# Performance work log

Measured on AMD Instinct MI355X. Metric: run time of the kernel, lower is better.

## Reference

```python
import jax, jax.numpy as jnp
import numpy as np

N_NODES = 100000
N_EDGES = 1600000
C = 64       # in_channels == filters
K = 3        # Chebyshev order
EPS = 1e-5   # InstanceNorm eps


def setup_inputs() -> dict:
    key = jax.random.key(0)
    ks = jax.random.split(key, 8)
    x = jax.random.normal(ks[0], (N_NODES, C), dtype=jnp.float32)
    edge_index = jax.random.randint(ks[1], (2, N_EDGES), 0, N_NODES, dtype=jnp.int64)
    scale = 1.0 / np.sqrt(C)
    W1 = jax.random.normal(ks[2], (K, C, C), dtype=jnp.float32) * scale
    b1 = jnp.zeros((C,), dtype=jnp.float32)
    W2 = jax.random.normal(ks[3], (K, C, C), dtype=jnp.float32) * scale
    b2 = jnp.zeros((C,), dtype=jnp.float32)
    return {"x": x, "edge_index": edge_index, "W1": W1, "b1": b1, "W2": W2, "b2": b2}


def _cheb_conv(x, src, dst, w_edge, W, b, n):
    # PyG ChebConv, norm='sym', lambda_max=2: L_hat = -D^{-1/2} A D^{-1/2}
    def prop(h):  # h: [N, C] -> L_hat @ h via gather -> weight -> scatter-add
        return jax.ops.segment_sum(w_edge[:, None] * h[src], dst, num_segments=n)
    Tx0 = x
    Tx1 = prop(x)
    Tx2 = 2.0 * prop(Tx1) - Tx0
    return Tx0 @ W[0] + Tx1 @ W[1] + Tx2 @ W[2] + b


def _instance_norm(h):
    # PyG InstanceNorm (single graph, affine=False): normalize over nodes per channel
    m = h.mean(axis=0, keepdims=True)
    v = h.var(axis=0, keepdims=True)
    return (h - m) * jax.lax.rsqrt(v + EPS)


def reference(x, edge_index, W1, b1, W2, b2):
    n = x.shape[0]
    src, dst = edge_index[0], edge_index[1]
    ones = jnp.ones((src.shape[0],), dtype=x.dtype)
    deg = jax.ops.segment_sum(ones, dst, num_segments=n)
    safe = jnp.where(deg > 0, deg, 1.0)
    dinv = jnp.where(deg > 0, jax.lax.rsqrt(safe), 0.0)
    w_edge = -dinv[src] * dinv[dst]  # scaled-Laplacian edge weights
    h = _instance_norm(jax.nn.relu(_cheb_conv(x, src, dst, w_edge, W1, b1, n)))
    h = _instance_norm(jax.nn.relu(_cheb_conv(h, src, dst, w_edge, W2, b2, n)))
    return h
```

## Files before the change

kernel.cpp:

```cpp
#include <hip/hip_runtime.h>
#include <hip/hip_fp16.h>

#define NCH 64
#define EPS 1e-5f
#define SBANKS 32
#define BSHIFT 8
#define NHIST 256
#define BINCAP 3200
#define NBINMIN 512
#define PADRES 2048
#define RSHIFT 14
#define SRCMASK 0x1FFFFu
#define QW_SCALE 32767.0f
#define QW_INV (1.0f/32767.0f)

typedef _Float16 f16x8 __attribute__((ext_vector_type(8)));
typedef float f32x4 __attribute__((ext_vector_type(4)));

__global__ __launch_bounds__(256) void k_front(const float* __restrict__ x, __half* __restrict__ xh,
                                               int castTotal, int castB,
                                               const float* __restrict__ W1, _Float16* __restrict__ Wb1,
                                               const float* __restrict__ W2, _Float16* __restrict__ Wb2,
                                               const int* __restrict__ dst, int* __restrict__ cnt,
                                               int E, int per, int nbuck) {
    int bid = blockIdx.x;
    if (bid < castB) {
        int i = (bid * 256 + threadIdx.x) * 4;
        if (i < castTotal) {
            float4 f = *(const float4*)(x + i);
            __half2* o = (__half2*)(xh + i);
            o[0] = __floats2half2_rn(f.x, f.y);
            o[1] = __floats2half2_rn(f.z, f.w);
        }
        return;
    }
    if (bid < castB + 96) {
        int wb = bid - castB;
        const float* W = (wb < 48) ? W1 : W2;
        _Float16* Wb = (wb < 48) ? Wb1 : Wb2;
        int idx = (wb % 48) * 256 + threadIdx.x;
        int j = idx & 7;
        int lane = (idx >> 3) & 63;
        int tk = idx >> 9;
        int tile = tk / 6, kk = tk % 6;
        int k = kk * 32 + (lane >> 4) * 8 + j;
        int n = tile * 16 + (lane & 15);
        Wb[idx] = (_Float16)W[k * 64 + n];
        return;
    }
    __shared__ int lh[512];
    int hb = bid - castB - 96;
    for (int t = threadIdx.x; t < nbuck; t += 256) lh[t] = 0;
    __syncthreads();
    int lo = hb * per, hi = min(E, lo + per);
    for (int e = lo + threadIdx.x; e < hi; e += 256)
        atomicAdd(&lh[dst[e] >> BSHIFT], 1);
    __syncthreads();
    for (int t = threadIdx.x; t < nbuck; t += 256)
        if (lh[t]) atomicAdd(&cnt[t], lh[t]);
}

__global__ void k_bscan(const int* __restrict__ cnt, int* __restrict__ gbase,
                        int* __restrict__ gcur, int nbuck, int E) {
    __shared__ int s[512];
    int t = threadIdx.x;
    int v = (t < nbuck) ? cnt[t] : 0;
    s[t] = v;
    __syncthreads();
    for (int off = 1; off < 512; off <<= 1) {
        int add = (t >= off) ? s[t - off] : 0;
        __syncthreads();
        s[t] += add;
        __syncthreads();
    }
    if (t < nbuck) { int ex = s[t] - v; gbase[t] = ex; gcur[t] = ex; }
    if (t == 0) gbase[nbuck] = E;
}

__global__ __launch_bounds__(256) void k_bin(const int* __restrict__ src,
                                             const int* __restrict__ dst,
                                             int* __restrict__ gcur,
                                             int2* __restrict__ binned, int E, int per, int nbuck) {
    __shared__ int lh[512];
    __shared__ int lsc[512];
    __shared__ int lbase[512];
    __shared__ int lcur[512];
    __shared__ int2 sedge[BINCAP];
    int t = threadIdx.x;
    for (int i = t; i < 512; i += 256) lh[i] = 0;
    __syncthreads();
    int lo = blockIdx.x * per, hi = min(E, lo + per);
    for (int e = lo + t; e < hi; e += 256)
        atomicAdd(&lh[dst[e] >> BSHIFT], 1);
    __syncthreads();
    int v0 = lh[t], v1 = lh[t + 256];
    lsc[t] = v0; lsc[t + 256] = v1;
    __syncthreads();
    for (int off = 1; off < 512; off <<= 1) {
        int a0 = (t >= off) ? lsc[t - off] : 0;
        int a1 = (t + 256 >= off) ? lsc[t + 256 - off] : 0;
        __syncthreads();
        lsc[t] += a0; lsc[t + 256] += a1;
        __syncthreads();
    }
    lsc[t] -= v0; lsc[t + 256] -= v1;
    if (t < nbuck && v0) lbase[t] = atomicAdd(&gcur[t], v0);
    if (t + 256 < nbuck && v1) lbase[t + 256] = atomicAdd(&gcur[t + 256], v1);
    lcur[t] = lsc[t]; lcur[t + 256] = lsc[t + 256];
    __syncthreads();
    for (int e = lo + t; e < hi; e += 256) {
        int d = dst[e];
        int b = d >> BSHIFT;
        int pos = atomicAdd(&lcur[b], 1);
        sedge[pos] = make_int2(src[e], d);
    }
    __syncthreads();
    int cntE = hi - lo;
    for (int i = t; i < cntE; i += 256) {
        int2 sd = sedge[i];
        int b = sd.y >> BSHIFT;
        binned[lbase[b] + (i - lsc[b])] = sd;
    }
}

__global__ __launch_bounds__(256) void k_bucket(const int2* __restrict__ binned,
                                                const int* __restrict__ gbase,
                                                float* __restrict__ dinv,
                                                int2* __restrict__ rowinfo,
                                                unsigned int* __restrict__ csr, int N, int nbuck) {
    __shared__ int hist8[256 * 8];
    __shared__ int cur8[256 * 8];
    __shared__ int ldeg[256];
    __shared__ int ltmp[256];
    int b = blockIdx.x;
    int t = threadIdx.x;
    int nodeLo = b << BSHIFT;
    int nHere = min(256, N - nodeLo);
    int e0 = gbase[b], e1 = gbase[b + 1];
    int pb = (gbase[b] + b * PADRES + 7) & ~7;
    for (int i = t; i < 256 * 8; i += 256) hist8[i] = 0;
    __syncthreads();
    for (int e = e0 + t; e < e1; e += 256) {
        int2 sd = binned[e];
        atomicAdd(&hist8[((sd.y - nodeLo) << 3) + (sd.x >> RSHIFT)], 1);
    }
    __syncthreads();
    int c[8], deg = 0;
#pragma unroll
    for (int r = 0; r < 8; r++) { c[r] = hist8[(t << 3) + r]; deg += c[r]; }
    int pdeg = (deg + 7) & ~7;
    ldeg[t] = deg;
    if (t < nHere) dinv[nodeLo + t] = (deg > 0) ? rsqrtf((float)deg) : 0.0f;
    ltmp[t] = pdeg;
    __syncthreads();
    for (int off = 1; off < 256; off <<= 1) {
        int add = (t >= off) ? ltmp[t - off] : 0;
        __syncthreads();
        ltmp[t] += add;
        __syncthreads();
    }
    int lstart = ltmp[t] - pdeg;
    if (t < nHere) rowinfo[nodeLo + t] = make_int2(pb + lstart, pdeg);
    int run = lstart;
#pragma unroll
    for (int r = 0; r < 8; r++) { cur8[(t << 3) + r] = run; run += c[r]; }
    __syncthreads();
    for (int e = e0 + t; e < e1; e += 256) {
        int2 sd = binned[e];
        int dl = sd.y - nodeLo;
        int pos = atomicAdd(&cur8[(dl << 3) + (sd.x >> RSHIFT)], 1);
        unsigned int dd = (unsigned int)min(ldeg[dl], 32767);
        csr[pb + pos] = (unsigned int)sd.x | (dd << 17);
    }
    __syncthreads();
    if (t < nHere) {
        int d = ldeg[t];
        int pd = (d + 7) & ~7;
        if (pd > d) {
            unsigned int fill = (d > 0) ? (csr[pb + lstart] & SRCMASK) : 0u;
            for (int i = d; i < pd; i++) csr[pb + lstart + i] = fill;
        }
    }
}

__global__ void k_weights(unsigned int* __restrict__ csr, const float* __restrict__ dinv, int PE) {
    int e = blockIdx.x * blockDim.x + threadIdx.x;
    if (e < PE) {
        unsigned int v = csr[e];
        unsigned int d = v >> 17;
        if (d == 0) return;
        unsigned int s = v & SRCMASK;
        float aw = dinv[s] * rsqrtf((float)d);
        unsigned int qw = (unsigned int)(aw * QW_SCALE + 0.5f);
        csr[e] = s | (qw << 17);
    }
}


#define GATH(A0,A1,A2,A3,A4,A5,A6,A7, C0, C1) \
    A0 = *(const uint4*)(hb + (size_t)(C0.x & SRCMASK) * NCH); \
    A1 = *(const uint4*)(hb + (size_t)(C0.y & SRCMASK) * NCH); \
    A2 = *(const uint4*)(hb + (size_t)(C0.z & SRCMASK) * NCH); \
    A3 = *(const uint4*)(hb + (size_t)(C0.w & SRCMASK) * NCH); \
    A4 = *(const uint4*)(hb + (size_t)(C1.x & SRCMASK) * NCH); \
    A5 = *(const uint4*)(hb + (size_t)(C1.y & SRCMASK) * NCH); \
    A6 = *(const uint4*)(hb + (size_t)(C1.z & SRCMASK) * NCH); \
    A7 = *(const uint4*)(hb + (size_t)(C1.w & SRCMASK) * NCH);

#define FMA1(A, W) { \
    float2 f; \
    f = __half22float2(*(const __half2*)&A.x); acc[0] = fmaf(W, f.x, acc[0]); acc[1] = fmaf(W, f.y, acc[1]); \
    f = __half22float2(*(const __half2*)&A.y); acc[2] = fmaf(W, f.x, acc[2]); acc[3] = fmaf(W, f.y, acc[3]); \
    f = __half22float2(*(const __half2*)&A.z); acc[4] = fmaf(W, f.x, acc[4]); acc[5] = fmaf(W, f.y, acc[5]); \
    f = __half22float2(*(const __half2*)&A.w); acc[6] = fmaf(W, f.x, acc[6]); acc[7] = fmaf(W, f.y, acc[7]); }

#define FMA8(A0,A1,A2,A3,A4,A5,A6,A7, C0, C1) { \
    float w0 = -(float)(C0.x >> 17) * QW_INV; \
    float w1 = -(float)(C0.y >> 17) * QW_INV; \
    float w2 = -(float)(C0.z >> 17) * QW_INV; \
    float w3 = -(float)(C0.w >> 17) * QW_INV; \
    float w4 = -(float)(C1.x >> 17) * QW_INV; \
    float w5 = -(float)(C1.y >> 17) * QW_INV; \
    float w6 = -(float)(C1.z >> 17) * QW_INV; \
    float w7 = -(float)(C1.w >> 17) * QW_INV; \
    sw += ((w0 + w1) + (w2 + w3)) + ((w4 + w5) + (w6 + w7)); \
    FMA1(A0, w0) FMA1(A1, w1) FMA1(A2, w2) FMA1(A3, w3) \
    FMA1(A4, w4) FMA1(A5, w5) FMA1(A6, w6) FMA1(A7, w7) }

__global__ __launch_bounds__(256) void k_prop(const __half* __restrict__ h,
                                              const int2* __restrict__ rowinfo,
                                              const unsigned int* __restrict__ csr,
                                              const __half* __restrict__ tx0,
                                              __half* __restrict__ y, int N,
                                              const float* __restrict__ gbank,
                                              const float* __restrict__ tbank,
                                              float invN) {
    __shared__ float sm[64], sr[64];
    const float* bank = (gbank != nullptr) ? gbank : tbank;
    if (bank != nullptr) {
        int tt = threadIdx.x;
        if (tt < 64) {
            float S = 0.f, Q = 0.f;
            for (int k = 0; k < SBANKS; k++) {
                S += bank[k * 128 + tt];
                Q += bank[k * 128 + 64 + tt];
            }
            float m = S * invN;
            float var = Q * invN - m * m;
            sm[tt] = m;
            sr[tt] = rsqrtf(var + EPS);
        }
        __syncthreads();
    }
    int lane = threadIdx.x & 63;
    int wv = (blockIdx.x * 256 + threadIdx.x) >> 6;
    int g = lane >> 3, li = lane & 7;
    int node = wv * 8 + g;
    int e = 0, e1 = 0;
    if (node < N) {
        int2 info = rowinfo[node];
        e = info.x;
        e1 = info.x + info.y;
    }
    float acc[8] = {0.f, 0.f, 0.f, 0.f, 0.f, 0.f, 0.f, 0.f};
    float sw = 0.0f;
    const __half* hb = h + li * 8;
    uint4 c0, c1;
    if (e < e1) {
        c0 = *(const uint4*)(csr + e);
        c1 = *(const uint4*)(csr + e + 4);
    }
    for (; e < e1; e += 8) {
        int en = (e + 8 < e1) ? (e + 8) : e;
        uint4 n0 = *(const uint4*)(csr + en);
        uint4 n1 = *(const uint4*)(csr + en + 4);
        uint4 a0, a1, a2, a3, a4, a5, a6, a7;
        GATH(a0, a1, a2, a3, a4, a5, a6, a7, c0, c1);
        FMA8(a0, a1, a2, a3, a4, a5, a6, a7, c0, c1);
        c0 = n0; c1 = n1;
    }
    if (node >= N) return;
    if (gbank != nullptr) {
        float4 m0 = *(const float4*)(sm + li * 8);
        float4 m1 = *(const float4*)(sm + li * 8 + 4);
        float4 r0 = *(const float4*)(sr + li * 8);
        float4 r1 = *(const float4*)(sr + li * 8 + 4);
        acc[0] = r0.x * (acc[0] - m0.x * sw);
        acc[1] = r0.y * (acc[1] - m0.y * sw);
        acc[2] = r0.z * (acc[2] - m0.z * sw);
        acc[3] = r0.w * (acc[3] - m0.w * sw);
        acc[4] = r1.x * (acc[4] - m1.x * sw);
        acc[5] = r1.y * (acc[5] - m1.y * sw);
        acc[6] = r1.z * (acc[6] - m1.z * sw);
        acc[7] = r1.w * (acc[7] - m1.w * sw);
    }
    if (tx0 != nullptr) {
        uint4 tq = *(const uint4*)(tx0 + (size_t)node * NCH + li * 8);
        float tv[8];
        float2 f;
        f = __half22float2(*(__half2*)&tq.x); tv[0] = f.x; tv[1] = f.y;
        f = __half22float2(*(__half2*)&tq.y); tv[2] = f.x; tv[3] = f.y;
        f = __half22float2(*(__half2*)&tq.z); tv[4] = f.x; tv[5] = f.y;
        f = __half22float2(*(__half2*)&tq.w); tv[6] = f.x; tv[7] = f.y;
        if (tbank != nullptr) {
            float4 m0 = *(const float4*)(sm + li * 8);
            float4 m1 = *(const float4*)(sm + li * 8 + 4);
            float4 r0 = *(const float4*)(sr + li * 8);
            float4 r1 = *(const float4*)(sr + li * 8 + 4);
            tv[0] = (tv[0] - m0.x) * r0.x; tv[1] = (tv[1] - m0.y) * r0.y;
            tv[2] = (tv[2] - m0.z) * r0.z; tv[3] = (tv[3] - m0.w) * r0.w;
            tv[4] = (tv[4] - m1.x) * r1.x; tv[5] = (tv[5] - m1.y) * r1.y;
            tv[6] = (tv[6] - m1.z) * r1.z; tv[7] = (tv[7] - m1.w) * r1.w;
        }
#pragma unroll
        for (int j = 0; j < 8; j++) acc[j] = 2.0f * acc[j] - tv[j];
    }
    uint4 o;
    __half2 hh;
    hh = __floats2half2_rn(acc[0], acc[1]); o.x = *(unsigned int*)&hh;
    hh = __floats2half2_rn(acc[2], acc[3]); o.y = *(unsigned int*)&hh;
    hh = __floats2half2_rn(acc[4], acc[5]); o.z = *(unsigned int*)&hh;
    hh = __floats2half2_rn(acc[6], acc[7]); o.w = *(unsigned int*)&hh;
    *(uint4*)(y + (size_t)node * NCH + li * 8) = o;
}

template <typename TOUT>
__global__ __launch_bounds__(256) void k_dmm(const __half* __restrict__ tx0,
                                             const __half* __restrict__ tx1,
                                             const __half* __restrict__ tx2,
                                             const _Float16* __restrict__ Wb,
                                             const float* __restrict__ b,
                                             TOUT* __restrict__ out,
                                             float* __restrict__ statsP, int N,
                                             const float* __restrict__ tbank,
                                             float invN) {
    __shared__ float sred[64];
    __shared__ float sq[64];
    __shared__ float tm[64];
    __shared__ float tr[64];
    int t = threadIdx.x;
    int w = t >> 6;
    int lane = t & 63;
    if (t < 64) {
        sred[t] = 0.f; sq[t] = 0.f;
        if (tbank != nullptr) {
            float S = 0.f, Q = 0.f;
            for (int k = 0; k < SBANKS; k++) {
                S += tbank[k * 128 + t];
                Q += tbank[k * 128 + 64 + t];
            }
            float m = S * invN;
            float var = Q * invN - m * m;
            tm[t] = m;
            tr[t] = rsqrtf(var + EPS);
        }
    }
    __syncthreads();

    int nb16 = blockIdx.x * 64 + w * 16;
    int m = lane & 15, q = lane >> 4;
    int row = nb16 + m;
    int rowC = (row < N) ? row : 0;
    const __half* base0 = tx0 + (size_t)rowC * NCH;
    const __half* base1 = tx1 + (size_t)rowC * NCH;
    const __half* base2 = tx2 + (size_t)rowC * NCH;

    f32x4 acc[4];
#pragma unroll
    for (int tile = 0; tile < 4; tile++) acc[tile] = (f32x4){0.f, 0.f, 0.f, 0.f};

#pragma unroll
    for (int kk = 0; kk < 6; kk++) {
        const __half* ap = (kk < 2 ? base0 : (kk < 4 ? base1 : base2)) + (kk & 1) * 32 + q * 8;
        f16x8 a = *(const f16x8*)ap;
        if (kk < 2 && tbank != nullptr) {
            int cbase = (kk & 1) * 32 + q * 8;
#pragma unroll
            for (int j = 0; j < 8; j++) {
                float v = (float)a[j];
                a[j] = (_Float16)((v - tm[cbase + j]) * tr[cbase + j]);
            }
        }
#pragma unroll
        for (int tile = 0; tile < 4; tile++) {
            f16x8 bf = *(const f16x8*)(Wb + ((size_t)(tile * 6 + kk) * 64 + lane) * 8);
            acc[tile] = __builtin_amdgcn_mfma_f32_16x16x32_f16(a, bf, acc[tile], 0, 0, 0);
        }
    }

#pragma unroll
    for (int tile = 0; tile < 4; tile++) {
        int ch = tile * 16 + m;
        float bb = b[ch];
        float s = 0.f, qq = 0.f;
#pragma unroll
        for (int r = 0; r < 4; r++) {
            int node = nb16 + q * 4 + r;
            float v = fmaxf(acc[tile][r] + bb, 0.f);
            if (node < N) {
                out[(size_t)node * NCH + ch] = (TOUT)v;
                s += v;
                qq = fmaf(v, v, qq);
            }
        }
        s += __shfl_xor(s, 16, 64);  s += __shfl_xor(s, 32, 64);
        qq += __shfl_xor(qq, 16, 64); qq += __shfl_xor(qq, 32, 64);
        if (q == 0) { atomicAdd(&sred[ch], s); atomicAdd(&sq[ch], qq); }
    }
    __syncthreads();
    if (t < 64) {
        int bank = blockIdx.x & (SBANKS - 1);
        atomicAdd(&statsP[bank * 128 + t], sred[t]);
        atomicAdd(&statsP[bank * 128 + 64 + t], sq[t]);
    }
}

__global__ __launch_bounds__(256) void k_norm_hf(const __half* __restrict__ a, float* __restrict__ o,
                                                 const float* __restrict__ sbank, float invN,
                                                 int total8) {
    __shared__ float sm[64];
    __shared__ float sr[64];
    int t = threadIdx.x;
    if (t < 64) {
        float S = 0.f, Q = 0.f;
        for (int k = 0; k < SBANKS; k++) {
            S += sbank[k * 128 + t];
            Q += sbank[k * 128 + 64 + t];
        }
        float m = S * invN;
        float var = Q * invN - m * m;
        sm[t] = m;
        sr[t] = rsqrtf(var + EPS);
    }
    __syncthreads();
    int i = blockIdx.x * 256 + t;
    if (i >= total8) return;
    int c0 = (i & 7) * 8;
    float4 m0 = *(const float4*)(sm + c0);
    float4 m1 = *(const float4*)(sm + c0 + 4);
    float4 r0 = *(const float4*)(sr + c0);
    float4 r1 = *(const float4*)(sr + c0 + 4);
    uint4 q = *(const uint4*)(a + (size_t)i * 8);
    float2 f;
    float4 o0, o1;
    f = __half22float2(*(__half2*)&q.x); o0.x = (f.x - m0.x) * r0.x; o0.y = (f.y - m0.y) * r0.y;
    f = __half22float2(*(__half2*)&q.y); o0.z = (f.x - m0.z) * r0.z; o0.w = (f.y - m0.w) * r0.w;
    f = __half22float2(*(__half2*)&q.z); o1.x = (f.x - m1.x) * r1.x; o1.y = (f.y - m1.y) * r1.y;
    f = __half22float2(*(__half2*)&q.w); o1.z = (f.x - m1.z) * r1.z; o1.w = (f.y - m1.w) * r1.w;
    *(float4*)(o + (size_t)i * 8) = o0;
    *(float4*)(o + (size_t)i * 8 + 4) = o1;
}

extern "C" void kernel_launch(void* const* d_in, const int* in_sizes, int n_in,
                              void* d_out, int out_size, void* d_ws, size_t ws_size,
                              hipStream_t stream) {
    const float* x  = (const float*)d_in[0];
    const int*   ei = (const int*)d_in[1];
    const float* W1 = (const float*)d_in[2];
    const float* b1 = (const float*)d_in[3];
    const float* W2 = (const float*)d_in[4];
    const float* b2 = (const float*)d_in[5];
    float* out = (float*)d_out;

    const int N = in_sizes[0] / NCH;
    const int E = in_sizes[1] / 2;
    const int* src = ei;
    const int* dst = ei + E;
    const int nbuck = (N + 255) >> BSHIFT;
    const int PE = E + nbuck * PADRES + 8;

    char* p = (char*)d_ws;
    auto alloc = [&](size_t bytes) {
        void* r = (void*)p;
        p += ((bytes + 255) / 256) * 256;
        return r;
    };
    float*  dinv     = (float*)alloc((size_t)131072 * 4);
    int2*   rowinfo  = (int2*)alloc((size_t)N * 8);
    unsigned int* csr = (unsigned int*)alloc((size_t)PE * 4);
    __half* xh       = (__half*)alloc((size_t)N * NCH * 2);
    __half* Tx1      = (__half*)alloc((size_t)N * NCH * 2);
    __half* Tx2      = (__half*)alloc((size_t)N * NCH * 2);
    __half* A        = (__half*)alloc((size_t)N * NCH * 2);
    __half* A2       = (__half*)alloc((size_t)N * NCH * 2);
    _Float16* Wb1    = (_Float16*)alloc(12288 * 2);
    _Float16* Wb2    = (_Float16*)alloc(12288 * 2);
    int*    gbase    = (int*)alloc((size_t)(nbuck + 1) * 4);
    int*    gcur     = (int*)alloc((size_t)nbuck * 4);
    const int statsFloats = SBANKS * 128 + 128;
    int*    cnt      = (int*)alloc((size_t)nbuck * 4 + (size_t)2 * statsFloats * 4);
    float*  stats1   = (float*)(cnt + nbuck);
    float*  stats2   = stats1 + statsFloats;

    int2* binned = (int2*)Tx1;

    hipMemsetAsync(cnt, 0, (size_t)nbuck * 4 + (size_t)2 * statsFloats * 4, stream);

    const int TB = 256;
    int nbin = (E + BINCAP - 1) / BINCAP;
    if (nbin < NBINMIN) nbin = NBINMIN;
    const int perBin = (E + nbin - 1) / nbin;
    const int perH = (E + NHIST - 1) / NHIST;
    const int castTotal = N * NCH;
    const int castB = (castTotal / 4 + TB - 1) / TB;
    k_front<<<castB + 96 + NHIST, TB, 0, stream>>>(x, xh, castTotal, castB,
                                                   W1, Wb1, W2, Wb2,
                                                   dst, cnt, E, perH, nbuck);
    k_bscan<<<1, 512, 0, stream>>>(cnt, gbase, gcur, nbuck, E);
    k_bin<<<nbin, TB, 0, stream>>>(src, dst, gcur, binned, E, perBin, nbuck);
    k_bucket<<<nbuck, TB, 0, stream>>>(binned, gbase, dinv, rowinfo, csr, N, nbuck);
    k_weights<<<(PE + TB - 1) / TB, TB, 0, stream>>>(csr, dinv, PE);

    const int propWaves = (N + 7) / 8;
    const int propBlocks = (propWaves + 3) / 4;
    const int dmmBlocks = (N + 63) / 64;
    const int total8 = (N * NCH) / 8;
    const int normBlocks = (total8 + TB - 1) / TB;
    const float invN = 1.0f / (float)N;

    k_prop<<<propBlocks, TB, 0, stream>>>(xh, rowinfo, csr, nullptr, Tx1, N, nullptr, nullptr, invN);
    k_prop<<<propBlocks, TB, 0, stream>>>(Tx1, rowinfo, csr, xh, Tx2, N, nullptr, nullptr, invN);
    k_dmm<__half><<<dmmBlocks, TB, 0, stream>>>(xh, Tx1, Tx2, Wb1, b1, A, stats1, N, nullptr, invN);

    k_prop<<<propBlocks, TB, 0, stream>>>(A, rowinfo, csr, nullptr, Tx1, N, stats1, nullptr, invN);
    k_prop<<<propBlocks, TB, 0, stream>>>(Tx1, rowinfo, csr, A, Tx2, N, nullptr, stats1, invN);
    k_dmm<__half><<<dmmBlocks, TB, 0, stream>>>(A, Tx1, Tx2, Wb2, b2, A2, stats2, N, stats1, invN);
    k_norm_hf<<<normBlocks, TB, 0, stream>>>(A2, out, stats2, invN, total8);
}
```

Before: 324.5 us.

## Compute degrees in binning pass and fold edge-weight quantization into bucket kernel

The binning kernel now counts per-node degree with global atomics, and a small kernel turns the degrees into dinv before bucketing. The bucket kernel then writes quantized edge weights straight into the CSR, which removes the separate full pass over the padded edge array. Binning also drops its shared-memory staging and prefix scan: it uses a fixed 1024 blocks and scatters edges directly with local atomic cursors. The costs are global atomics on a degree array, a larger memset, and less coalesced writes to the binned array.

After: 395.6 us. 1.22x slower.

```diff
diff --git a/kernel.cpp b/kernel.cpp
--- a/kernel.cpp
+++ b/kernel.cpp
@@ -6,8 +6,7 @@
 #define SBANKS 32
 #define BSHIFT 8
 #define NHIST 256
-#define BINCAP 3200
-#define NBINMIN 512
+#define NBIN 1024
 #define PADRES 2048
 #define RSHIFT 14
 #define SRCMASK 0x1FFFFu
@@ -80,57 +79,49 @@
 __global__ __launch_bounds__(256) void k_bin(const int* __restrict__ src,
                                              const int* __restrict__ dst,
                                              int* __restrict__ gcur,
+                                             int* __restrict__ deg,
                                              int2* __restrict__ binned, int E, int per, int nbuck) {
     __shared__ int lh[512];
-    __shared__ int lsc[512];
     __shared__ int lbase[512];
-    __shared__ int lcur[512];
-    __shared__ int2 sedge[BINCAP];
     int t = threadIdx.x;
-    for (int i = t; i < 512; i += 256) lh[i] = 0;
+    lh[t] = 0; lh[t + 256] = 0;
     __syncthreads();
     int lo = blockIdx.x * per, hi = min(E, lo + per);
-    for (int e = lo + t; e < hi; e += 256)
-        atomicAdd(&lh[dst[e] >> BSHIFT], 1);
-    __syncthreads();
-    int v0 = lh[t], v1 = lh[t + 256];
-    lsc[t] = v0; lsc[t + 256] = v1;
-    __syncthreads();
-    for (int off = 1; off < 512; off <<= 1) {
-        int a0 = (t >= off) ? lsc[t - off] : 0;
-        int a1 = (t + 256 >= off) ? lsc[t + 256 - off] : 0;
-        __syncthreads();
-        lsc[t] += a0; lsc[t + 256] += a1;
-        __syncthreads();
-    }
-    lsc[t] -= v0; lsc[t + 256] -= v1;
-    if (t < nbuck && v0) lbase[t] = atomicAdd(&gcur[t], v0);
-    if (t + 256 < nbuck && v1) lbase[t + 256] = atomicAdd(&gcur[t + 256], v1);
-    lcur[t] = lsc[t]; lcur[t + 256] = lsc[t + 256];
+    for (int e = lo + t; e < hi; e += 256) {
+        int d = dst[e];
+        atomicAdd(&lh[d >> BSHIFT], 1);
+        atomicAdd(&deg[d], 1);
+    }
+    __syncthreads();
+    int c0 = lh[t], c1 = lh[t + 256];
+    if (c0) lbase[t] = atomicAdd(&gcur[t], c0);
+    if (c1) lbase[t + 256] = atomicAdd(&gcur[t + 256], c1);
+    lh[t] = 0; lh[t + 256] = 0;
     __syncthreads();
     for (int e = lo + t; e < hi; e += 256) {
         int d = dst[e];
         int b = d >> BSHIFT;
-        int pos = atomicAdd(&lcur[b], 1);
-        sedge[pos] = make_int2(src[e], d);
-    }
-    __syncthreads();
-    int cntE = hi - lo;
-    for (int i = t; i < cntE; i += 256) {
-        int2 sd = sedge[i];
-        int b = sd.y >> BSHIFT;
-        binned[lbase[b] + (i - lsc[b])] = sd;
+        int pos = atomicAdd(&lh[b], 1);
+        binned[lbase[b] + pos] = make_int2(src[e], d);
+    }
+}
+
+__global__ void k_dinv(const int* __restrict__ deg, float* __restrict__ dinv, int N) {
+    int i = blockIdx.x * blockDim.x + threadIdx.x;
+    if (i < N) {
+        int d = deg[i];
+        dinv[i] = (d > 0) ? rsqrtf((float)d) : 0.0f;
     }
 }
 
 __global__ __launch_bounds__(256) void k_bucket(const int2* __restrict__ binned,
                                                 const int* __restrict__ gbase,
-                                                float* __restrict__ dinv,
+                                                const float* __restrict__ dinv,
                                                 int2* __restrict__ rowinfo,
                                                 unsigned int* __restrict__ csr, int N, int nbuck) {
     __shared__ int hist8[256 * 8];
     __shared__ int cur8[256 * 8];
-    __shared__ int ldeg[256];
+    __shared__ float ldr[256];
     __shared__ int ltmp[256];
     int b = blockIdx.x;
     int t = threadIdx.x;
@@ -149,8 +140,7 @@
 #pragma unroll
     for (int r = 0; r < 8; r++) { c[r] = hist8[(t << 3) + r]; deg += c[r]; }
     int pdeg = (deg + 7) & ~7;
-    ldeg[t] = deg;
-    if (t < nHere) dinv[nodeLo + t] = (deg > 0) ? rsqrtf((float)deg) : 0.0f;
+    ldr[t] = (deg > 0) ? rsqrtf((float)deg) : 0.0f;
     ltmp[t] = pdeg;
     __syncthreads();
     for (int off = 1; off < 256; off <<= 1) {
@@ -169,30 +159,20 @@
         int2 sd = binned[e];
         int dl = sd.y - nodeLo;
         int pos = atomicAdd(&cur8[(dl << 3) + (sd.x >> RSHIFT)], 1);
-        unsigned int dd = (unsigned int)min(ldeg[dl], 32767);
-        csr[pb + pos] = (unsigned int)sd.x | (dd << 17);
+        float aw = dinv[sd.x] * ldr[dl];
+        unsigned int qw = (unsigned int)(aw * QW_SCALE + 0.5f);
+        csr[pb + pos] = (unsigned int)sd.x | (qw << 17);
     }
     __syncthreads();
     if (t < nHere) {
-        int d = ldeg[t];
+        int d = 0;
+#pragma unroll
+        for (int r = 0; r < 8; r++) d += c[r];
         int pd = (d + 7) & ~7;
         if (pd > d) {
             unsigned int fill = (d > 0) ? (csr[pb + lstart] & SRCMASK) : 0u;
             for (int i = d; i < pd; i++) csr[pb + lstart + i] = fill;
         }
-    }
-}
-
-__global__ void k_weights(unsigned int* __restrict__ csr, const float* __restrict__ dinv, int PE) {
-    int e = blockIdx.x * blockDim.x + threadIdx.x;
-    if (e < PE) {
-        unsigned int v = csr[e];
-        unsigned int d = v >> 17;
-        if (d == 0) return;
-        unsigned int s = v & SRCMASK;
-        float aw = dinv[s] * rsqrtf((float)d);
-        unsigned int qw = (unsigned int)(aw * QW_SCALE + 0.5f);
-        csr[e] = s | (qw << 17);
     }
 }
 
@@ -475,7 +455,7 @@
         p += ((bytes + 255) / 256) * 256;
         return r;
     };
-    float*  dinv     = (float*)alloc((size_t)131072 * 4);
+    float*  dinv     = (float*)alloc((size_t)N * 4);
     int2*   rowinfo  = (int2*)alloc((size_t)N * 8);
     unsigned int* csr = (unsigned int*)alloc((size_t)PE * 4);
     __half* xh       = (__half*)alloc((size_t)N * NCH * 2);
@@ -488,18 +468,18 @@
     int*    gbase    = (int*)alloc((size_t)(nbuck + 1) * 4);
     int*    gcur     = (int*)alloc((size_t)nbuck * 4);
     const int statsFloats = SBANKS * 128 + 128;
-    int*    cnt      = (int*)alloc((size_t)nbuck * 4 + (size_t)2 * statsFloats * 4);
-    float*  stats1   = (float*)(cnt + nbuck);
+    const size_t zbytes = (size_t)nbuck * 4 + (size_t)N * 4 + (size_t)2 * statsFloats * 4;
+    int*    cnt      = (int*)alloc(zbytes);
+    int*    deg      = cnt + nbuck;
+    float*  stats1   = (float*)(deg + N);
     float*  stats2   = stats1 + statsFloats;
 
     int2* binned = (int2*)Tx1;
 
-    hipMemsetAsync(cnt, 0, (size_t)nbuck * 4 + (size_t)2 * statsFloats * 4, stream);
+    hipMemsetAsync(cnt, 0, zbytes, stream);
 
     const int TB = 256;
-    int nbin = (E + BINCAP - 1) / BINCAP;
-    if (nbin < NBINMIN) nbin = NBINMIN;
-    const int perBin = (E + nbin - 1) / nbin;
+    const int perBin = (E + NBIN - 1) / NBIN;
     const int perH = (E + NHIST - 1) / NHIST;
     const int castTotal = N * NCH;
     const int castB = (castTotal / 4 + TB - 1) / TB;
@@ -507,9 +487,9 @@
                                                    W1, Wb1, W2, Wb2,
                                                    dst, cnt, E, perH, nbuck);
     k_bscan<<<1, 512, 0, stream>>>(cnt, gbase, gcur, nbuck, E);
-    k_bin<<<nbin, TB, 0, stream>>>(src, dst, gcur, binned, E, perBin, nbuck);
+    k_bin<<<NBIN, TB, 0, stream>>>(src, dst, gcur, deg, binned, E, perBin, nbuck);
+    k_dinv<<<(N + TB - 1) / TB, TB, 0, stream>>>(deg, dinv, N);
     k_bucket<<<nbuck, TB, 0, stream>>>(binned, gbase, dinv, rowinfo, csr, N, nbuck);
-    k_weights<<<(PE + TB - 1) / TB, TB, 0, stream>>>(csr, dinv, PE);
 
     const int propWaves = (N + 7) / 8;
     const int propBlocks = (propWaves + 3) / 4;
```
